# Kernel optimization log

Measured on AMD Instinct MI355X. Metric: run time of the kernel, lower is better.

## Reference

```python
import jax, jax.numpy as jnp
import numpy as np

N = 50000      # nodes
E = 800000     # edges per meta-path
P = 3          # meta-paths
IN = 128       # in_size
OUT = 64       # out_size per head
H = 4          # heads
HID = 128      # semantic-attention hidden
NEG_SLOPE = 0.2


def setup_inputs() -> dict:
    key = jax.random.key(0)
    ks = jax.random.split(key, 8)
    h = jax.random.normal(ks[0], (N, IN), jnp.float32)
    edges = jax.random.randint(ks[1], (P, 2, E), 0, N, dtype=jnp.int32)  # [P, (src,dst), E]
    fc_w = jax.random.normal(ks[2], (P, IN, H * OUT), jnp.float32) * 0.05
    attn_l = jax.random.normal(ks[3], (P, H, OUT), jnp.float32) * 0.05
    attn_r = jax.random.normal(ks[4], (P, H, OUT), jnp.float32) * 0.05
    w1 = jax.random.normal(ks[5], (H * OUT, HID), jnp.float32) * 0.05
    b1 = jnp.zeros((HID,), jnp.float32)
    w2 = jax.random.normal(ks[6], (HID,), jnp.float32) * 0.05
    return {"h": h, "edges": edges, "fc_w": fc_w, "attn_l": attn_l,
            "attn_r": attn_r, "w1": w1, "b1": b1, "w2": w2}


def _gat(h, edge, fc_w, al, ar):
    # One GATConv (DGL semantics, eval mode: dropout off, no residual/bias).
    src, dst = edge[0], edge[1]
    feat = (h @ fc_w).reshape(N, H, OUT)                 # [N,H,D]
    el = jnp.einsum('nhd,hd->nh', feat, al)              # [N,H]
    er = jnp.einsum('nhd,hd->nh', feat, ar)
    e = jax.nn.leaky_relu(el[src] + er[dst], NEG_SLOPE)  # [E,H]
    # edge softmax over incoming edges of each dst node
    m = jax.ops.segment_max(e, dst, num_segments=N)      # [N,H]
    m = jnp.where(jnp.isfinite(m), m, 0.0)               # empty segments -> 0
    ex = jnp.exp(e - m[dst])
    s = jax.ops.segment_sum(ex, dst, num_segments=N)     # [N,H]
    alpha = ex / s[dst]                                  # [E,H]
    msg = feat[src] * alpha[:, :, None]                  # [E,H,D]
    rst = jax.ops.segment_sum(msg, dst, num_segments=N)  # [N,H,D]
    return jax.nn.elu(rst).reshape(N, H * OUT)


def reference(h, edges, fc_w, attn_l, attn_r, w1, b1, w2):
    # per-meta-path GAT embeddings -> [N, P, H*OUT]
    z = jnp.stack([_gat(h, edges[i], fc_w[i], attn_l[i], attn_r[i])
                   for i in range(P)], axis=1)
    # semantic attention: Linear -> tanh -> Linear(no bias) -> softmax over P
    w = jnp.tanh(z @ w1 + b1) @ w2                       # [N,P]
    beta = jax.nn.softmax(w, axis=1)[:, :, None]         # [N,P,1]
    return (beta * z).sum(axis=1)                        # [N, H*OUT]
```

## Files before the change

### kernel.cpp

```cpp
#include <hip/hip_runtime.h>
#include <hip/hip_bf16.h>
#include <hip/hip_fp16.h>

#define N_NODES 50000
#define N_EDGES 800000
#define N_PATHS 3
#define IN_F    128
#define HO      256
#define N_HEADS 4
#define HID     128

#define BLK_PER_PATH 32
#define EDGES_PER_HB 25000
#define HIST_BLOCKS  (N_PATHS * BLK_PER_PATH)
#define NPACK        12500
#define FEAT_RB      782
#define SCAT_BLOCKS  2344
#define FEAT_ELEMS   ((size_t)N_NODES * HO)

typedef __bf16 bf16;
typedef __bf16 bf16x8 __attribute__((ext_vector_type(8)));
typedef float  f32x4  __attribute__((ext_vector_type(4)));
typedef unsigned short u16;
typedef unsigned char  u8;
typedef unsigned int   u32;

__global__ __launch_bounds__(256) void k_prep(const float* __restrict__ fc_w,
                                              bf16* __restrict__ fcwT) {
    int g = blockIdx.x * 256 + threadIdx.x;
    int p = g >> 15, r = g & 32767;
    int col = r & 255, k = r >> 8;
    fcwT[(size_t)p * 32768 + col * IN_F + k] = (bf16)fc_w[(size_t)p * 32768 + k * HO + col];
}

__global__ __launch_bounds__(256) void k_hist(const int* __restrict__ edges,
                                              u32* __restrict__ cnt32,
                                              u8* __restrict__ lrank) {
    __shared__ u32 hist[NPACK];
    const int b = blockIdx.x;
    const int p = b / BLK_PER_PATH, blk = b - p * BLK_PER_PATH;
    const int t = threadIdx.x;
    for (int i = t; i < NPACK; i += 256) hist[i] = 0;
    __syncthreads();

    const int* dstp = edges + (size_t)p * 2 * N_EDGES + N_EDGES + blk * EDGES_PER_HB;
    u8* lr = lrank + (size_t)p * N_EDGES + blk * EDGES_PER_HB;
    for (int q = t; q < EDGES_PER_HB / 4; q += 256) {
        int4 d4 = ((const int4*)dstp)[q];
        u32 o0 = atomicAdd(&hist[d4.x >> 2], 1u << ((d4.x & 3) * 8));
        u32 o1 = atomicAdd(&hist[d4.y >> 2], 1u << ((d4.y & 3) * 8));
        u32 o2 = atomicAdd(&hist[d4.z >> 2], 1u << ((d4.z & 3) * 8));
        u32 o3 = atomicAdd(&hist[d4.w >> 2], 1u << ((d4.w & 3) * 8));
        uchar4 r4;
        r4.x = (u8)(o0 >> ((d4.x & 3) * 8));
        r4.y = (u8)(o1 >> ((d4.y & 3) * 8));
        r4.z = (u8)(o2 >> ((d4.z & 3) * 8));
        r4.w = (u8)(o3 >> ((d4.w & 3) * 8));
        ((uchar4*)lr)[q] = r4;
    }
    __syncthreads();
    u32* out = cnt32 + (size_t)b * NPACK;
    for (int i = t; i < NPACK; i += 256) out[i] = hist[i];
}

__global__ __launch_bounds__(256) void k_base(u32* __restrict__ cnt32,
                                              int* __restrict__ deg) {
    int g = blockIdx.x * 256 + threadIdx.x;
    if (g >= N_PATHS * NPACK) return;
    int p = g / NPACK, q = g - p * NPACK;
    u32 s0 = 0, s1 = 0, s2 = 0, s3 = 0;
#pragma unroll
    for (int blk = 0; blk < BLK_PER_PATH; ++blk) {
        size_t idx = (size_t)(p * BLK_PER_PATH + blk) * NPACK + q;
        u32 c = cnt32[idx];
        cnt32[idx] = s0 | (s1 << 8) | (s2 << 16) | (s3 << 24);
        s0 += c & 0xff; s1 += (c >> 8) & 0xff; s2 += (c >> 16) & 0xff; s3 += c >> 24;
    }
    int4 d4 = {(int)s0, (int)s1, (int)s2, (int)s3};
    *(int4*)(deg + (size_t)p * N_NODES + 4 * q) = d4;
}

__global__ __launch_bounds__(1024) void k_scan(const int* __restrict__ deg,
                                               int* __restrict__ rowptr) {
    __shared__ int part[1024];
    const int p = blockIdx.x;
    const int* dg = deg + p * N_NODES;
    int* rp = rowptr + p * (N_NODES + 1);

    const int tid = threadIdx.x;
    const int CH = (N_NODES + 1023) / 1024;
    const int start = tid * CH;
    int s = 0;
    for (int i = 0; i < CH; ++i) { int idx = start + i; if (idx < N_NODES) s += dg[idx]; }
    part[tid] = s;
    __syncthreads();
    for (int off = 1; off < 1024; off <<= 1) {
        int v = (tid >= off) ? part[tid - off] : 0;
        __syncthreads();
        part[tid] += v;
        __syncthreads();
    }
    int excl = (tid == 0) ? 0 : part[tid - 1];
    for (int i = 0; i < CH; ++i) {
        int idx = start + i;
        if (idx < N_NODES) { rp[idx] = excl; excl += dg[idx]; }
    }
    if (tid == 1023) rp[N_NODES] = N_EDGES;
}

__device__ __forceinline__ void scatter_role(int b, const int* __restrict__ edges,
                                             const u8* __restrict__ lrank,
                                             const u32* __restrict__ cnt32,
                                             const int* __restrict__ rowptr,
                                             u16* __restrict__ csr) {
    int gt = b * 256 + threadIdx.x;
    if (gt >= (N_PATHS * N_EDGES) / 4) return;
    int base = gt * 4;
    int p = base / N_EDGES, e = base - p * N_EDGES;
    const int blk = e / EDGES_PER_HB;
    const int* ep = edges + (size_t)p * 2 * N_EDGES;
    int4 s4 = *(const int4*)(ep + e);
    int4 d4 = *(const int4*)(ep + N_EDGES + e);
    uchar4 r4 = *(const uchar4*)(lrank + base);
    const int* rp = rowptr + p * (N_NODES + 1);
    const u32* bb = cnt32 + (size_t)(p * BLK_PER_PATH + blk) * NPACK;
    u16* c = csr + (size_t)p * N_EDGES;
    int p0 = rp[d4.x] + ((bb[d4.x >> 2] >> ((d4.x & 3) * 8)) & 0xff) + r4.x;
    int p1 = rp[d4.y] + ((bb[d4.y >> 2] >> ((d4.y & 3) * 8)) & 0xff) + r4.y;
    int p2 = rp[d4.z] + ((bb[d4.z >> 2] >> ((d4.z & 3) * 8)) & 0xff) + r4.z;
    int p3 = rp[d4.w] + ((bb[d4.w >> 2] >> ((d4.w & 3) * 8)) & 0xff) + r4.w;
    c[p0] = (u16)s4.x; c[p1] = (u16)s4.y; c[p2] = (u16)s4.z; c[p3] = (u16)s4.w;
}

__device__ __forceinline__ void feat_role(int rb, const float* __restrict__ h,
                                          const bf16* __restrict__ fcwT,
                                          const float* __restrict__ al,
                                          const float* __restrict__ ar,
                                          __half* __restrict__ featAll,
                                          float* __restrict__ elAll,
                                          float* __restrict__ erAll) {
    const int t = threadIdx.x, w = t >> 6, l = t & 63, lo = l & 15, hi = l >> 4;
    const int arow = rb * 64 + w * 16 + lo;
    const int crow = rb * 64 + w * 16 + hi * 4;

    bf16x8 afr[4];
    if (arow < N_NODES) {
        const float* hp = h + (size_t)arow * IN_F;
#pragma unroll
        for (int ks = 0; ks < 4; ++ks) {
            float4 f0 = *(const float4*)(hp + ks * 32 + hi * 8);
            float4 f1 = *(const float4*)(hp + ks * 32 + hi * 8 + 4);
            bf16x8 a;
            a[0]=(bf16)f0.x; a[1]=(bf16)f0.y; a[2]=(bf16)f0.z; a[3]=(bf16)f0.w;
            a[4]=(bf16)f1.x; a[5]=(bf16)f1.y; a[6]=(bf16)f1.z; a[7]=(bf16)f1.w;
            afr[ks] = a;
        }
    } else {
#pragma unroll
        for (int ks = 0; ks < 4; ++ks) { bf16x8 a = {}; afr[ks] = a; }
    }

    for (int p = 0; p < N_PATHS; ++p) {
        __half* feat = featAll + (size_t)p * FEAT_ELEMS;
        const float* alp = al + p * HO;
        const float* arp = ar + p * HO;
        float* elA = elAll + (size_t)p * N_NODES * 4;
        float* erA = erAll + (size_t)p * N_NODES * 4;
#pragma unroll
        for (int ch = 0; ch < 2; ++ch) {
            const bf16* W = fcwT + (size_t)p * 32768 + (size_t)ch * 128 * IN_F;
            f32x4 acc[8];
#pragma unroll
            for (int c = 0; c < 8; ++c) { f32x4 zz = {0.f,0.f,0.f,0.f}; acc[c] = zz; }
#pragma unroll
            for (int ctl = 0; ctl < 8; ++ctl) {
                const bf16* wp = W + (size_t)(ctl * 16 + lo) * IN_F + hi * 8;
                f32x4 a = acc[ctl];
#pragma unroll
                for (int ks = 0; ks < 4; ++ks)
                    a = __builtin_amdgcn_mfma_f32_16x16x32_bf16(afr[ks], *(const bf16x8*)(wp + ks * 32), a, 0, 0, 0);
                acc[ctl] = a;
            }
            float elP[2][4] = {{0}}, erP[2][4] = {{0}};
#pragma unroll
            for (int ctl = 0; ctl < 8; ++ctl) {
                const int gcol = ch * 128 + ctl * 16 + lo;
                const float av = alp[gcol], bv = arp[gcol];
                const int hl = ctl >> 2;
#pragma unroll
                for (int rr = 0; rr < 4; ++rr) {
                    float v = acc[ctl][rr];
                    elP[hl][rr] = fmaf(v, av, elP[hl][rr]);
                    erP[hl][rr] = fmaf(v, bv, erP[hl][rr]);
                    if (crow + rr < N_NODES)
                        feat[(size_t)(crow + rr) * HO + gcol] = __float2half(v);
                }
            }
#pragma unroll
            for (int hl = 0; hl < 2; ++hl)
#pragma unroll
                for (int rr = 0; rr < 4; ++rr) {
                    float v = elP[hl][rr], u = erP[hl][rr];
#pragma unroll
                    for (int m = 1; m <= 8; m <<= 1) {
                        v += __shfl_xor(v, m, 64);
                        u += __shfl_xor(u, m, 64);
                    }
                    elP[hl][rr] = v; erP[hl][rr] = u;
                }
            if (lo == 0) {
#pragma unroll
                for (int rr = 0; rr < 4; ++rr) {
                    if (crow + rr < N_NODES) {
                        *(float2*)&elA[(crow + rr) * 4 + ch * 2] = make_float2(elP[0][rr], elP[1][rr]);
                        *(float2*)&erA[(crow + rr) * 4 + ch * 2] = make_float2(erP[0][rr], erP[1][rr]);
                    }
                }
            }
        }
    }
}

__global__ __launch_bounds__(256, 4) void k_fs(const int* __restrict__ edges,
                                               const u8* __restrict__ lrank,
                                               const u32* __restrict__ cnt32,
                                               const int* __restrict__ rowptr,
                                               u16* __restrict__ csr,
                                               const float* __restrict__ h,
                                               const bf16* __restrict__ fcwT,
                                               const float* __restrict__ al,
                                               const float* __restrict__ ar,
                                               __half* __restrict__ featAll,
                                               float* __restrict__ elAll,
                                               float* __restrict__ erAll) {
    const int bid = blockIdx.x;
    if (bid < SCAT_BLOCKS)
        scatter_role(bid, edges, lrank, cnt32, rowptr, csr);
    else
        feat_role(bid - SCAT_BLOCKS, h, fcwT, al, ar, featAll, elAll, erAll);
}

__global__ __launch_bounds__(256) void k_gather3(const u16* __restrict__ csrAll,
                                                 const int* __restrict__ rowptrAll,
                                                 const float4* __restrict__ elAll,
                                                 const float4* __restrict__ erAll,
                                                 const __half* __restrict__ featAll,
                                                 bf16* __restrict__ z) {
    __shared__ int     off_lds[4][64];
    __shared__ __half2 a_lds[4][64][4];
    const int pb = blockIdx.x;
    const int p  = pb / (N_NODES / 4);
    const int nb = pb - p * (N_NODES / 4);
    const u16*    csr    = csrAll + (size_t)p * N_EDGES;
    const int*    rowptr = rowptrAll + p * (N_NODES + 1);
    const float4* el4    = elAll + (size_t)p * N_NODES;
    const float4* er4    = erAll + (size_t)p * N_NODES;
    const __half* feat   = featAll + (size_t)p * FEAT_ELEMS;

    const int wid = threadIdx.x >> 6, l = threadIdx.x & 63;
    const int n = nb * 4 + wid;
    const int half = l >> 5, c = l & 31, hh = c >> 3;

    const int b0 = rowptr[n], b1 = rowptr[n + 1];
    const float4 er_n = er4[n];

    __half2 acc0 = __float2half2_rn(0.f), acc1 = acc0, acc2 = acc0, acc3 = acc0;
    float4 den = {0.f, 0.f, 0.f, 0.f};

    for (int base = b0; base < b1; base += 64) {
        const int cnt = min(64, b1 - base);
        if (l < cnt) {
            int sv = csr[base + l];
            off_lds[wid][l] = sv * HO;
            float4 e = el4[sv];
            float vx = e.x + er_n.x, vy = e.y + er_n.y,
                  vz = e.z + er_n.z, vw = e.w + er_n.w;
            vx = (vx >= 0.f) ? vx : 0.2f * vx;
            vy = (vy >= 0.f) ? vy : 0.2f * vy;
            vz = (vz >= 0.f) ? vz : 0.2f * vz;
            vw = (vw >= 0.f) ? vw : 0.2f * vw;
            float ex = __expf(vx), ey = __expf(vy), ez = __expf(vz), ew = __expf(vw);
            den.x += ex; den.y += ey; den.z += ez; den.w += ew;
            a_lds[wid][l][0] = __float2half2_rn(ex);
            a_lds[wid][l][1] = __float2half2_rn(ey);
            a_lds[wid][l][2] = __float2half2_rn(ez);
            a_lds[wid][l][3] = __float2half2_rn(ew);
        }
        for (int i2 = 0; i2 < cnt; i2 += 2) {
            const int e = i2 + half;
            if (e < cnt) {
                const int off = off_lds[wid][e];
                const __half2 a2 = a_lds[wid][e][hh];
                const uint4 u = *(const uint4*)(feat + off + c * 8);
                acc0 = __hfma2(__builtin_bit_cast(__half2, u.x), a2, acc0);
                acc1 = __hfma2(__builtin_bit_cast(__half2, u.y), a2, acc1);
                acc2 = __hfma2(__builtin_bit_cast(__half2, u.z), a2, acc2);
                acc3 = __hfma2(__builtin_bit_cast(__half2, u.w), a2, acc3);
            }
        }
    }

    float s[8];
    { float2 f0 = __half22float2(acc0), f1 = __half22float2(acc1),
             f2 = __half22float2(acc2), f3 = __half22float2(acc3);
      s[0]=f0.x; s[1]=f0.y; s[2]=f1.x; s[3]=f1.y; s[4]=f2.x; s[5]=f2.y; s[6]=f3.x; s[7]=f3.y; }
#pragma unroll
    for (int j = 0; j < 8; ++j) s[j] += __shfl_xor(s[j], 32, 64);
#pragma unroll
    for (int off = 32; off; off >>= 1) {
        den.x += __shfl_xor(den.x, off, 64);
        den.y += __shfl_xor(den.y, off, 64);
        den.z += __shfl_xor(den.z, off, 64);
        den.w += __shfl_xor(den.w, off, 64);
    }
    const float d = (hh == 0) ? den.x : (hh == 1) ? den.y : (hh == 2) ? den.z : den.w;
    const float inv = (d > 0.f) ? 1.f / d : 0.f;
    if (half == 0) {
        bf16x8 ov;
#pragma unroll
        for (int j = 0; j < 8; ++j) {
            float v = s[j] * inv;
            v = (v > 0.f) ? v : expm1f(v);
            ov[j] = (bf16)v;
        }
        *(bf16x8*)(z + (size_t)n * (N_PATHS * HO) + p * HO + c * 8) = ov;
    }
}

__global__ __launch_bounds__(256) void k_semout(const bf16* __restrict__ z,
                                                const float* __restrict__ w1,
                                                const float* __restrict__ b1,
                                                const float* __restrict__ w2,
                                                float* __restrict__ out) {
    __shared__ bf16  zs[48 * 264];
    __shared__ float psem[4][48];
    __shared__ float betas[16][4];

    const int t = threadIdx.x, w = t >> 6, l = t & 63;
    const int lo = l & 15, hi = l >> 4;
    const int n0 = blockIdx.x * 16;

    bf16x8 bfr[2][8];
#pragma unroll
    for (int ct = 0; ct < 2; ++ct) {
        const int j = (2 * w + ct) * 16 + lo;
#pragma unroll
        for (int s = 0; s < 8; ++s) {
            const int k0 = s * 32 + hi * 8;
            bf16x8 b;
#pragma unroll
            for (int i = 0; i < 8; ++i) b[i] = (bf16)w1[(k0 + i) * HID + j];
            bfr[ct][s] = b;
        }
    }

    const uint4* zg4 = (const uint4*)(z + (size_t)n0 * (N_PATHS * HO));
    for (int i = t; i < 1536; i += 256) {
        uint4 v = zg4[i];
        int r = i >> 5, cin = (i & 31) * 8;
        *(uint4*)&zs[r * 264 + cin] = v;
    }
    __syncthreads();

    f32x4 acc[2][3];
#pragma unroll
    for (int ct = 0; ct < 2; ++ct)
#pragma unroll
        for (int m = 0; m < 3; ++m) { f32x4 zz = {0.f,0.f,0.f,0.f}; acc[ct][m] = zz; }

    for (int s = 0; s < 8; ++s) {
#pragma unroll
        for (int m = 0; m < 3; ++m) {
            bf16x8 a = *(const bf16x8*)&zs[(m * 16 + lo) * 264 + s * 32 + hi * 8];
            acc[0][m] = __builtin_amdgcn_mfma_f32_16x16x32_bf16(a, bfr[0][s], acc[0][m], 0, 0, 0);
            acc[1][m] = __builtin_amdgcn_mfma_f32_16x16x32_bf16(a, bfr[1][s], acc[1][m], 0, 0, 0);
        }
    }

    const int j0 = (2 * w + 0) * 16 + lo;
    const int j1 = (2 * w + 1) * 16 + lo;
    const float b1_0 = b1[j0], w2_0 = w2[j0];
    const float b1_1 = b1[j1], w2_1 = w2[j1];
#pragma unroll
    for (int m = 0; m < 3; ++m) {
#pragma unroll
        for (int r = 0; r < 4; ++r) {
// ... 16 lines not shown
        float is = 1.f / (e0 + e1 + e2);
        betas[t][0] = e0 * is; betas[t][1] = e1 * is; betas[t][2] = e2 * is;
    }
    __syncthreads();
    for (int i = 0; i < 16; ++i) {
        float bb0 = betas[i][0], bb1 = betas[i][1], bb2 = betas[i][2];
        float o = bb0 * (float)zs[(3 * i + 0) * 264 + t]
                + bb1 * (float)zs[(3 * i + 1) * 264 + t]
                + bb2 * (float)zs[(3 * i + 2) * 264 + t];
        out[(size_t)(n0 + i) * HO + t] = o;
    }
}

static inline size_t align256(size_t x) { return (x + 255) & ~(size_t)255; }

extern "C" void kernel_launch(void* const* d_in, const int* in_sizes, int n_in,
                              void* d_out, int out_size, void* d_ws, size_t ws_size,
                              hipStream_t stream) {
    const float* h     = (const float*)d_in[0];
    const int*   edges = (const int*)d_in[1];
    const float* fc_w  = (const float*)d_in[2];
    const float* al    = (const float*)d_in[3];
    const float* ar    = (const float*)d_in[4];
    const float* w1    = (const float*)d_in[5];
    const float* b1    = (const float*)d_in[6];
    const float* w2    = (const float*)d_in[7];
    float* out = (float*)d_out;

    char* base = (char*)d_ws;
    size_t off = 0;
    auto carve = [&](size_t bytes) -> char* {
        char* p = base + off; off = align256(off + bytes); return p;
    };
    bf16*   zbuf   = (bf16*)carve((size_t)N_NODES * N_PATHS * HO * 2);
    __half* feat   = (__half*)carve((size_t)N_PATHS * FEAT_ELEMS * 2);
    bf16*   fcwT   = (bf16*)carve((size_t)N_PATHS * IN_F * HO * 2);
    float*  el     = (float*)carve((size_t)N_PATHS * N_NODES * 4 * 4);
    float*  er     = (float*)carve((size_t)N_PATHS * N_NODES * 4 * 4);
    int*    deg    = (int*)carve((size_t)N_PATHS * N_NODES * 4);
    int*    rowptr = (int*)carve((size_t)N_PATHS * (N_NODES + 1) * 4);
    u8*     lrank  = (u8*)carve((size_t)N_PATHS * N_EDGES);
    u16*    csr    = (u16*)carve((size_t)N_PATHS * N_EDGES * 2);
    u32*    cnt32  = (u32*)carve((size_t)HIST_BLOCKS * NPACK * 4);
    (void)ws_size; (void)in_sizes; (void)n_in; (void)out_size;

    k_prep<<<384, 256, 0, stream>>>(fc_w, fcwT);
    k_hist<<<HIST_BLOCKS, 256, 0, stream>>>(edges, cnt32, lrank);
    k_base<<<(N_PATHS * NPACK + 255) / 256, 256, 0, stream>>>(cnt32, deg);
    k_scan<<<N_PATHS, 1024, 0, stream>>>(deg, rowptr);
    k_fs<<<SCAT_BLOCKS + FEAT_RB, 256, 0, stream>>>(
        edges, lrank, cnt32, rowptr, csr, h, fcwT, al, ar, feat, el, er);
    k_gather3<<<N_PATHS * (N_NODES / 4), 256, 0, stream>>>(
        csr, rowptr, (const float4*)el, (const float4*)er, feat, zbuf);
    k_semout<<<N_NODES / 16, 256, 0, stream>>>(zbuf, w1, b1, w2, out);
}
```

Measured before the change: 492.3 us.

## Precompute edge attention in CSR scatter and co-schedule feature GEMM with histogram

The feature GEMM now runs in the same launch as the dst histogram instead of alongside the CSR scatter. The scatter kernel runs after the features exist. It computes each edge's leaky-relu exp weights and stores a 16-byte record (src offset plus fp16 weights) at the edge's CSR position. The gather kernel then reads these precomputed records and no longer does the random el/er lookups and exp itself. It also unrolls the aggregation loop to two edges per half-wave, for more loads in flight. The cost is scatter traffic of 16 B per edge instead of 2 B, and the 48 KB histogram LDS allocation is now shared with the feature blocks, which may reduce their occupancy.

Result: slower. 515.1 us (+4.6%).

```diff
diff --git a/kernel.cpp b/kernel.cpp
--- a/kernel.cpp
+++ b/kernel.cpp
@@ -25,6 +25,8 @@
 typedef unsigned char  u8;
 typedef unsigned int   u32;
 
+struct EdEnt { int off; __half2 a; };
+
 __global__ __launch_bounds__(256) void k_prep(const float* __restrict__ fc_w,
                                               bf16* __restrict__ fcwT) {
     int g = blockIdx.x * 256 + threadIdx.x;
@@ -33,11 +35,9 @@
     fcwT[(size_t)p * 32768 + col * IN_F + k] = (bf16)fc_w[(size_t)p * 32768 + k * HO + col];
 }
 
-__global__ __launch_bounds__(256) void k_hist(const int* __restrict__ edges,
-                                              u32* __restrict__ cnt32,
-                                              u8* __restrict__ lrank) {
-    __shared__ u32 hist[NPACK];
-    const int b = blockIdx.x;
+__device__ __forceinline__ void hist_role(int b, const int* __restrict__ edges,
+                                          u32* __restrict__ cnt32, u8* __restrict__ lrank,
+                                          u32* hist) {
     const int p = b / BLK_PER_PATH, blk = b - p * BLK_PER_PATH;
     const int t = threadIdx.x;
     for (int i = t; i < NPACK; i += 256) hist[i] = 0;
@@ -63,6 +63,113 @@
     for (int i = t; i < NPACK; i += 256) out[i] = hist[i];
 }
 
+__device__ __forceinline__ void feat_role(int rb, const float* __restrict__ h,
+                                          const bf16* __restrict__ fcwT,
+                                          const float* __restrict__ al,
+                                          const float* __restrict__ ar,
+                                          __half* __restrict__ featAll,
+                                          float* __restrict__ elAll,
+                                          float* __restrict__ erAll) {
+    const int t = threadIdx.x, w = t >> 6, l = t & 63, lo = l & 15, hi = l >> 4;
+    const int arow = rb * 64 + w * 16 + lo;
+    const int crow = rb * 64 + w * 16 + hi * 4;
+
+    bf16x8 afr[4];
+    if (arow < N_NODES) {
+        const float* hp = h + (size_t)arow * IN_F;
+#pragma unroll
+        for (int ks = 0; ks < 4; ++ks) {
+            float4 f0 = *(const float4*)(hp + ks * 32 + hi * 8);
+            float4 f1 = *(const float4*)(hp + ks * 32 + hi * 8 + 4);
+            bf16x8 a;
+            a[0]=(bf16)f0.x; a[1]=(bf16)f0.y; a[2]=(bf16)f0.z; a[3]=(bf16)f0.w;
+            a[4]=(bf16)f1.x; a[5]=(bf16)f1.y; a[6]=(bf16)f1.z; a[7]=(bf16)f1.w;
+            afr[ks] = a;
+        }
+    } else {
+#pragma unroll
+        for (int ks = 0; ks < 4; ++ks) { bf16x8 a = {}; afr[ks] = a; }
+    }
+
+    for (int p = 0; p < N_PATHS; ++p) {
+        __half* feat = featAll + (size_t)p * FEAT_ELEMS;
+        const float* alp = al + p * HO;
+        const float* arp = ar + p * HO;
+        float* elA = elAll + (size_t)p * N_NODES * 4;
+        float* erA = erAll + (size_t)p * N_NODES * 4;
+#pragma unroll
+        for (int ch = 0; ch < 2; ++ch) {
+            const bf16* W = fcwT + (size_t)p * 32768 + (size_t)ch * 128 * IN_F;
+            f32x4 acc[8];
+#pragma unroll
+            for (int c = 0; c < 8; ++c) { f32x4 zz = {0.f,0.f,0.f,0.f}; acc[c] = zz; }
+#pragma unroll
+            for (int ctl = 0; ctl < 8; ++ctl) {
+                const bf16* wp = W + (size_t)(ctl * 16 + lo) * IN_F + hi * 8;
+                f32x4 a = acc[ctl];
+#pragma unroll
+                for (int ks = 0; ks < 4; ++ks)
+                    a = __builtin_amdgcn_mfma_f32_16x16x32_bf16(afr[ks], *(const bf16x8*)(wp + ks * 32), a, 0, 0, 0);
+                acc[ctl] = a;
+            }
+            float elP[2][4] = {{0}}, erP[2][4] = {{0}};
+#pragma unroll
+            for (int ctl = 0; ctl < 8; ++ctl) {
+                const int gcol = ch * 128 + ctl * 16 + lo;
+                const float av = alp[gcol], bv = arp[gcol];
+                const int hl = ctl >> 2;
+#pragma unroll
+                for (int rr = 0; rr < 4; ++rr) {
+                    float v = acc[ctl][rr];
+                    elP[hl][rr] = fmaf(v, av, elP[hl][rr]);
+                    erP[hl][rr] = fmaf(v, bv, erP[hl][rr]);
+                    if (crow + rr < N_NODES)
+                        feat[(size_t)(crow + rr) * HO + gcol] = __float2half(v);
+                }
+            }
+#pragma unroll
+            for (int hl = 0; hl < 2; ++hl)
+#pragma unroll
+                for (int rr = 0; rr < 4; ++rr) {
+                    float v = elP[hl][rr], u = erP[hl][rr];
+#pragma unroll
+                    for (int m = 1; m <= 8; m <<= 1) {
+                        v += __shfl_xor(v, m, 64);
+                        u += __shfl_xor(u, m, 64);
+                    }
+                    elP[hl][rr] = v; erP[hl][rr] = u;
+                }
+            if (lo == 0) {
+#pragma unroll
+                for (int rr = 0; rr < 4; ++rr) {
+                    if (crow + rr < N_NODES) {
+                        *(float2*)&elA[(crow + rr) * 4 + ch * 2] = make_float2(elP[0][rr], elP[1][rr]);
+                        *(float2*)&erA[(crow + rr) * 4 + ch * 2] = make_float2(erP[0][rr], erP[1][rr]);
+                    }
+                }
+            }
+        }
+    }
+}
+
+__global__ __launch_bounds__(256) void k_hf(const int* __restrict__ edges,
+                                            u32* __restrict__ cnt32,
+                                            u8* __restrict__ lrank,
+                                            const float* __restrict__ h,
+                                            const bf16* __restrict__ fcwT,
+                                            const float* __restrict__ al,
+                                            const float* __restrict__ ar,
+                                            __half* __restrict__ featAll,
+                                            float* __restrict__ elAll,
+                                            float* __restrict__ erAll) {
+    __shared__ u32 hist[NPACK];
+    const int bid = blockIdx.x;
+    if (bid < HIST_BLOCKS)
+        hist_role(bid, edges, cnt32, lrank, hist);
+    else
+        feat_role(bid - HIST_BLOCKS, h, fcwT, al, ar, featAll, elAll, erAll);
+}
+
 __global__ __launch_bounds__(256) void k_base(u32* __restrict__ cnt32,
                                               int* __restrict__ deg) {
     int g = blockIdx.x * 256 + threadIdx.x;
@@ -108,12 +215,14 @@
     if (tid == 1023) rp[N_NODES] = N_EDGES;
 }
 
-__device__ __forceinline__ void scatter_role(int b, const int* __restrict__ edges,
-                                             const u8* __restrict__ lrank,
-                                             const u32* __restrict__ cnt32,
-                                             const int* __restrict__ rowptr,
-                                             u16* __restrict__ csr) {
-    int gt = b * 256 + threadIdx.x;
+__global__ __launch_bounds__(256) void k_scata(const int* __restrict__ edges,
+                                               const u8* __restrict__ lrank,
+                                               const u32* __restrict__ cnt32,
+                                               const int* __restrict__ rowptr,
+                                               const float4* __restrict__ elAll,
+                                               const float4* __restrict__ erAll,
+                                               uint4* __restrict__ csrE) {
+    int gt = blockIdx.x * 256 + threadIdx.x;
     if (gt >= (N_PATHS * N_EDGES) / 4) return;
     int base = gt * 4;
     int p = base / N_EDGES, e = base - p * N_EDGES;
@@ -124,145 +233,51 @@
     uchar4 r4 = *(const uchar4*)(lrank + base);
     const int* rp = rowptr + p * (N_NODES + 1);
     const u32* bb = cnt32 + (size_t)(p * BLK_PER_PATH + blk) * NPACK;
-    u16* c = csr + (size_t)p * N_EDGES;
-    int p0 = rp[d4.x] + ((bb[d4.x >> 2] >> ((d4.x & 3) * 8)) & 0xff) + r4.x;
-    int p1 = rp[d4.y] + ((bb[d4.y >> 2] >> ((d4.y & 3) * 8)) & 0xff) + r4.y;
-    int p2 = rp[d4.z] + ((bb[d4.z >> 2] >> ((d4.z & 3) * 8)) & 0xff) + r4.z;
-    int p3 = rp[d4.w] + ((bb[d4.w >> 2] >> ((d4.w & 3) * 8)) & 0xff) + r4.w;
-    c[p0] = (u16)s4.x; c[p1] = (u16)s4.y; c[p2] = (u16)s4.z; c[p3] = (u16)s4.w;
-}
-
-__device__ __forceinline__ void feat_role(int rb, const float* __restrict__ h,
-                                          const bf16* __restrict__ fcwT,
-                                          const float* __restrict__ al,
-                                          const float* __restrict__ ar,
-                                          __half* __restrict__ featAll,
-                                          float* __restrict__ elAll,
-                                          float* __restrict__ erAll) {
-    const int t = threadIdx.x, w = t >> 6, l = t & 63, lo = l & 15, hi = l >> 4;
-    const int arow = rb * 64 + w * 16 + lo;
-    const int crow = rb * 64 + w * 16 + hi * 4;
-
-    bf16x8 afr[4];
-    if (arow < N_NODES) {
-        const float* hp = h + (size_t)arow * IN_F;
-#pragma unroll
-        for (int ks = 0; ks < 4; ++ks) {
-            float4 f0 = *(const float4*)(hp + ks * 32 + hi * 8);
-            float4 f1 = *(const float4*)(hp + ks * 32 + hi * 8 + 4);
-            bf16x8 a;
-            a[0]=(bf16)f0.x; a[1]=(bf16)f0.y; a[2]=(bf16)f0.z; a[3]=(bf16)f0.w;
-            a[4]=(bf16)f1.x; a[5]=(bf16)f1.y; a[6]=(bf16)f1.z; a[7]=(bf16)f1.w;
-            afr[ks] = a;
-        }
-    } else {
-#pragma unroll
-        for (int ks = 0; ks < 4; ++ks) { bf16x8 a = {}; afr[ks] = a; }
-    }
-
-    for (int p = 0; p < N_PATHS; ++p) {
-        __half* feat = featAll + (size_t)p * FEAT_ELEMS;
-        const float* alp = al + p * HO;
-        const float* arp = ar + p * HO;
-        float* elA = elAll + (size_t)p * N_NODES * 4;
-        float* erA = erAll + (size_t)p * N_NODES * 4;
-#pragma unroll
-        for (int ch = 0; ch < 2; ++ch) {
-            const bf16* W = fcwT + (size_t)p * 32768 + (size_t)ch * 128 * IN_F;
-            f32x4 acc[8];
-#pragma unroll
-            for (int c = 0; c < 8; ++c) { f32x4 zz = {0.f,0.f,0.f,0.f}; acc[c] = zz; }
-#pragma unroll
-            for (int ctl = 0; ctl < 8; ++ctl) {
-                const bf16* wp = W + (size_t)(ctl * 16 + lo) * IN_F + hi * 8;
-                f32x4 a = acc[ctl];
-#pragma unroll
-                for (int ks = 0; ks < 4; ++ks)
-                    a = __builtin_amdgcn_mfma_f32_16x16x32_bf16(afr[ks], *(const bf16x8*)(wp + ks * 32), a, 0, 0, 0);
-                acc[ctl] = a;
-            }
-            float elP[2][4] = {{0}}, erP[2][4] = {{0}};
-#pragma unroll
-            for (int ctl = 0; ctl < 8; ++ctl) {
-                const int gcol = ch * 128 + ctl * 16 + lo;
-                const float av = alp[gcol], bv = arp[gcol];
-                const int hl = ctl >> 2;
-#pragma unroll
-                for (int rr = 0; rr < 4; ++rr) {
-                    float v = acc[ctl][rr];
-                    elP[hl][rr] = fmaf(v, av, elP[hl][rr]);
-                    erP[hl][rr] = fmaf(v, bv, erP[hl][rr]);
-                    if (crow + rr < N_NODES)
-                        feat[(size_t)(crow + rr) * HO + gcol] = __float2half(v);
-                }
-            }
-#pragma unroll
-            for (int hl = 0; hl < 2; ++hl)
-#pragma unroll
-                for (int rr = 0; rr < 4; ++rr) {
-                    float v = elP[hl][rr], u = erP[hl][rr];
-#pragma unroll
-                    for (int m = 1; m <= 8; m <<= 1) {
-                        v += __shfl_xor(v, m, 64);
-                        u += __shfl_xor(u, m, 64);
-                    }
-                    elP[hl][rr] = v; erP[hl][rr] = u;
-                }
-            if (lo == 0) {
-#pragma unroll
-                for (int rr = 0; rr < 4; ++rr) {
-                    if (crow + rr < N_NODES) {
-                        *(float2*)&elA[(crow + rr) * 4 + ch * 2] = make_float2(elP[0][rr], elP[1][rr]);
-                        *(float2*)&erA[(crow + rr) * 4 + ch * 2] = make_float2(erP[0][rr], erP[1][rr]);
-                    }
-                }
-            }
-        }
-    }
-}
-
-__global__ __launch_bounds__(256, 4) void k_fs(const int* __restrict__ edges,
-                                               const u8* __restrict__ lrank,
-                                               const u32* __restrict__ cnt32,
-                                               const int* __restrict__ rowptr,
-                                               u16* __restrict__ csr,
-                                               const float* __restrict__ h,
-                                               const bf16* __restrict__ fcwT,
-                                               const float* __restrict__ al,
-                                               const float* __restrict__ ar,
-                                               __half* __restrict__ featAll,
-                                               float* __restrict__ elAll,
-                                               float* __restrict__ erAll) {
-    const int bid = blockIdx.x;
-    if (bid < SCAT_BLOCKS)
-        scatter_role(bid, edges, lrank, cnt32, rowptr, csr);
-    else
-        feat_role(bid - SCAT_BLOCKS, h, fcwT, al, ar, featAll, elAll, erAll);
-}
-
-__global__ __launch_bounds__(256) void k_gather3(const u16* __restrict__ csrAll,
+    const float4* el4 = elAll + (size_t)p * N_NODES;
+    const float4* er4 = erAll + (size_t)p * N_NODES;
+    uint4* cE = csrE + (size_t)p * N_EDGES;
+
+    int ss[4] = {s4.x, s4.y, s4.z, s4.w};
+    int dd[4] = {d4.x, d4.y, d4.z, d4.w};
+    int rr[4] = {r4.x, r4.y, r4.z, r4.w};
+#pragma unroll
+    for (int j = 0; j < 4; ++j) {
+        const int s = ss[j], d = dd[j];
+        const int pos = rp[d] + (int)((bb[d >> 2] >> ((d & 3) * 8)) & 0xff) + rr[j];
+        float4 a = el4[s], b = er4[d];
+        float vx = a.x + b.x, vy = a.y + b.y, vz = a.z + b.z, vw = a.w + b.w;
+        vx = (vx >= 0.f) ? vx : 0.2f * vx;
+        vy = (vy >= 0.f) ? vy : 0.2f * vy;
+        vz = (vz >= 0.f) ? vz : 0.2f * vz;
+        vw = (vw >= 0.f) ? vw : 0.2f * vw;
+        __half2 h01 = __floats2half2_rn(__expf(vx), __expf(vy));
+        __half2 h23 = __floats2half2_rn(__expf(vz), __expf(vw));
+        uint4 entry;
+        entry.x = (u32)(s * HO);
+        entry.y = __builtin_bit_cast(u32, h01);
+        entry.z = __builtin_bit_cast(u32, h23);
+        entry.w = 0;
+        cE[pos] = entry;
+    }
+}
+
+__global__ __launch_bounds__(256) void k_gather3(const uint4* __restrict__ csrEAll,
                                                  const int* __restrict__ rowptrAll,
-                                                 const float4* __restrict__ elAll,
-                                                 const float4* __restrict__ erAll,
                                                  const __half* __restrict__ featAll,
                                                  bf16* __restrict__ z) {
-    __shared__ int     off_lds[4][64];
-    __shared__ __half2 a_lds[4][64][4];
+    __shared__ EdEnt ed[4][64][4];
     const int pb = blockIdx.x;
     const int p  = pb / (N_NODES / 4);
     const int nb = pb - p * (N_NODES / 4);
-    const u16*    csr    = csrAll + (size_t)p * N_EDGES;
-    const int*    rowptr = rowptrAll + p * (N_NODES + 1);
-    const float4* el4    = elAll + (size_t)p * N_NODES;
-    const float4* er4    = erAll + (size_t)p * N_NODES;
-    const __half* feat   = featAll + (size_t)p * FEAT_ELEMS;
+    const uint4* cE    = csrEAll + (size_t)p * N_EDGES;
+    const int* rowptr  = rowptrAll + p * (N_NODES + 1);
+    const __half* feat = featAll + (size_t)p * FEAT_ELEMS;
 
     const int wid = threadIdx.x >> 6, l = threadIdx.x & 63;
     const int n = nb * 4 + wid;
     const int half = l >> 5, c = l & 31, hh = c >> 3;
 
     const int b0 = rowptr[n], b1 = rowptr[n + 1];
-    const float4 er_n = er4[n];
 
     __half2 acc0 = __float2half2_rn(0.f), acc1 = acc0, acc2 = acc0, acc3 = acc0;
     float4 den = {0.f, 0.f, 0.f, 0.f};
@@ -270,32 +285,42 @@
     for (int base = b0; base < b1; base += 64) {
         const int cnt = min(64, b1 - base);
         if (l < cnt) {
-            int sv = csr[base + l];
-            off_lds[wid][l] = sv * HO;
-            float4 e = el4[sv];
-            float vx = e.x + er_n.x, vy = e.y + er_n.y,
-                  vz = e.z + er_n.z, vw = e.w + er_n.w;
-            vx = (vx >= 0.f) ? vx : 0.2f * vx;
-            vy = (vy >= 0.f) ? vy : 0.2f * vy;
-            vz = (vz >= 0.f) ? vz : 0.2f * vz;
-            vw = (vw >= 0.f) ? vw : 0.2f * vw;
-            float ex = __expf(vx), ey = __expf(vy), ez = __expf(vz), ew = __expf(vw);
-            den.x += ex; den.y += ey; den.z += ez; den.w += ew;
-            a_lds[wid][l][0] = __float2half2_rn(ex);
-            a_lds[wid][l][1] = __float2half2_rn(ey);
-            a_lds[wid][l][2] = __float2half2_rn(ez);
-            a_lds[wid][l][3] = __float2half2_rn(ew);
-        }
-        for (int i2 = 0; i2 < cnt; i2 += 2) {
+            uint4 m = cE[base + l];
+            __half2 h01 = __builtin_bit_cast(__half2, m.y);
+            __half2 h23 = __builtin_bit_cast(__half2, m.z);
+            float2 f01 = __half22float2(h01);
+            float2 f23 = __half22float2(h23);
+            den.x += f01.x; den.y += f01.y; den.z += f23.x; den.w += f23.y;
+            EdEnt* ep = ed[wid][l];
+            ep[0].off = (int)m.x; ep[0].a = __half2half2(__low2half(h01));
+            ep[1].off = (int)m.x; ep[1].a = __half2half2(__high2half(h01));
+            ep[2].off = (int)m.x; ep[2].a = __half2half2(__low2half(h23));
+            ep[3].off = (int)m.x; ep[3].a = __half2half2(__high2half(h23));
+        }
+        int i2 = 0;
+        for (; i2 + 4 <= cnt; i2 += 4) {
+            EdEnt e1 = ed[wid][i2 + half][hh];
+            EdEnt e2 = ed[wid][i2 + 2 + half][hh];
+            const uint4 u1 = *(const uint4*)(feat + e1.off + c * 8);
+            const uint4 u2 = *(const uint4*)(feat + e2.off + c * 8);
+            acc0 = __hfma2(__builtin_bit_cast(__half2, u1.x), e1.a, acc0);
+            acc1 = __hfma2(__builtin_bit_cast(__half2, u1.y), e1.a, acc1);
+            acc2 = __hfma2(__builtin_bit_cast(__half2, u1.z), e1.a, acc2);
+            acc3 = __hfma2(__builtin_bit_cast(__half2, u1.w), e1.a, acc3);
+            acc0 = __hfma2(__builtin_bit_cast(__half2, u2.x), e2.a, acc0);
+            acc1 = __hfma2(__builtin_bit_cast(__half2, u2.y), e2.a, acc1);
+            acc2 = __hfma2(__builtin_bit_cast(__half2, u2.z), e2.a, acc2);
+            acc3 = __hfma2(__builtin_bit_cast(__half2, u2.w), e2.a, acc3);
+        }
+        for (; i2 < cnt; i2 += 2) {
             const int e = i2 + half;
             if (e < cnt) {
-                const int off = off_lds[wid][e];
-                const __half2 a2 = a_lds[wid][e][hh];
-                const uint4 u = *(const uint4*)(feat + off + c * 8);
-                acc0 = __hfma2(__builtin_bit_cast(__half2, u.x), a2, acc0);
-                acc1 = __hfma2(__builtin_bit_cast(__half2, u.y), a2, acc1);
-                acc2 = __hfma2(__builtin_bit_cast(__half2, u.z), a2, acc2);
-                acc3 = __hfma2(__builtin_bit_cast(__half2, u.w), a2, acc3);
+                EdEnt e1 = ed[wid][e][hh];
+                const uint4 u = *(const uint4*)(feat + e1.off + c * 8);
+                acc0 = __hfma2(__builtin_bit_cast(__half2, u.x), e1.a, acc0);
+                acc1 = __hfma2(__builtin_bit_cast(__half2, u.y), e1.a, acc1);
+                acc2 = __hfma2(__builtin_bit_cast(__half2, u.z), e1.a, acc2);
+                acc3 = __hfma2(__builtin_bit_cast(__half2, u.w), e1.a, acc3);
             }
         }
     }
@@ -436,23 +461,23 @@
     };
     bf16*   zbuf   = (bf16*)carve((size_t)N_NODES * N_PATHS * HO * 2);
     __half* feat   = (__half*)carve((size_t)N_PATHS * FEAT_ELEMS * 2);
+    uint4*  csrE   = (uint4*)carve((size_t)N_PATHS * N_EDGES * 16);
     bf16*   fcwT   = (bf16*)carve((size_t)N_PATHS * IN_F * HO * 2);
     float*  el     = (float*)carve((size_t)N_PATHS * N_NODES * 4 * 4);
     float*  er     = (float*)carve((size_t)N_PATHS * N_NODES * 4 * 4);
     int*    deg    = (int*)carve((size_t)N_PATHS * N_NODES * 4);
     int*    rowptr = (int*)carve((size_t)N_PATHS * (N_NODES + 1) * 4);
     u8*     lrank  = (u8*)carve((size_t)N_PATHS * N_EDGES);
-    u16*    csr    = (u16*)carve((size_t)N_PATHS * N_EDGES * 2);
     u32*    cnt32  = (u32*)carve((size_t)HIST_BLOCKS * NPACK * 4);
     (void)ws_size; (void)in_sizes; (void)n_in; (void)out_size;
 
     k_prep<<<384, 256, 0, stream>>>(fc_w, fcwT);
-    k_hist<<<HIST_BLOCKS, 256, 0, stream>>>(edges, cnt32, lrank);
+    k_hf<<<HIST_BLOCKS + FEAT_RB, 256, 0, stream>>>(
+        edges, cnt32, lrank, h, fcwT, al, ar, feat, el, er);
     k_base<<<(N_PATHS * NPACK + 255) / 256, 256, 0, stream>>>(cnt32, deg);
     k_scan<<<N_PATHS, 1024, 0, stream>>>(deg, rowptr);
-    k_fs<<<SCAT_BLOCKS + FEAT_RB, 256, 0, stream>>>(
-        edges, lrank, cnt32, rowptr, csr, h, fcwT, al, ar, feat, el, er);
-    k_gather3<<<N_PATHS * (N_NODES / 4), 256, 0, stream>>>(
-        csr, rowptr, (const float4*)el, (const float4*)er, feat, zbuf);
+    k_scata<<<SCAT_BLOCKS, 256, 0, stream>>>(
+        edges, lrank, cnt32, rowptr, (const float4*)el, (const float4*)er, csrE);
+    k_gather3<<<N_PATHS * (N_NODES / 4), 256, 0, stream>>>(csrE, rowptr, feat, zbuf);
     k_semout<<<N_NODES / 16, 256, 0, stream>>>(zbuf, w1, b1, w2, out);
 }
```

## Restructure pipeline: fuse histogram with feature GEMM, overlap per-path scatter with gather

Applied to the files above, without the earlier changes.

The histogram pass now runs in the same launch as the feature projection, so both become independent blocks of one kernel. The CSR scatter for path p+1 now runs in the same launch as the aggregation for path p, split into per-path kernels that pipeline the scatter and gather stages. The gather inner loop is unrolled to issue two feature loads per lane per iteration, and its LDS attention layout is transposed. w1 is pre-transposed to bf16 in the prep kernel so semout can use vector loads. The cost is more launches, and the hist role's 50KB of shared memory may reduce occupancy of the feature blocks.

New measurement: 486.9 us. No clear change (-1.1%).

```diff
diff --git a/kernel.cpp b/kernel.cpp
--- a/kernel.cpp
+++ b/kernel.cpp
@@ -15,7 +15,8 @@
 #define HIST_BLOCKS  (N_PATHS * BLK_PER_PATH)
 #define NPACK        12500
 #define FEAT_RB      782
-#define SCAT_BLOCKS  2344
+#define SCAT_PP      782
+#define GATH_PP      12500
 #define FEAT_ELEMS   ((size_t)N_NODES * HO)
 
 typedef __bf16 bf16;
@@ -26,18 +27,26 @@
 typedef unsigned int   u32;
 
 __global__ __launch_bounds__(256) void k_prep(const float* __restrict__ fc_w,
-                                              bf16* __restrict__ fcwT) {
+                                              const float* __restrict__ w1,
+                                              bf16* __restrict__ fcwT,
+                                              bf16* __restrict__ w1T) {
     int g = blockIdx.x * 256 + threadIdx.x;
-    int p = g >> 15, r = g & 32767;
-    int col = r & 255, k = r >> 8;
-    fcwT[(size_t)p * 32768 + col * IN_F + k] = (bf16)fc_w[(size_t)p * 32768 + k * HO + col];
-}
-
-__global__ __launch_bounds__(256) void k_hist(const int* __restrict__ edges,
-                                              u32* __restrict__ cnt32,
-                                              u8* __restrict__ lrank) {
-    __shared__ u32 hist[NPACK];
-    const int b = blockIdx.x;
+    if (g < N_PATHS * IN_F * HO) {
+        int p = g >> 15, r = g & 32767;
+        int col = r & 255, k = r >> 8;
+        fcwT[(size_t)p * 32768 + col * IN_F + k] = (bf16)fc_w[(size_t)p * 32768 + k * HO + col];
+    } else {
+        int gg = g - N_PATHS * IN_F * HO;
+        if (gg < HO * HID) {
+            int k = gg & 255, j = gg >> 8;
+            w1T[(size_t)j * HO + k] = (bf16)w1[(size_t)k * HID + j];
+        }
+    }
+}
+
+__device__ __forceinline__ void hist_role(int b, const int* __restrict__ edges,
+                                          u32* __restrict__ cnt32, u8* __restrict__ lrank,
+                                          u32* hist) {
     const int p = b / BLK_PER_PATH, blk = b - p * BLK_PER_PATH;
     const int t = threadIdx.x;
     for (int i = t; i < NPACK; i += 256) hist[i] = 0;
@@ -63,75 +72,6 @@
     for (int i = t; i < NPACK; i += 256) out[i] = hist[i];
 }
 
-__global__ __launch_bounds__(256) void k_base(u32* __restrict__ cnt32,
-                                              int* __restrict__ deg) {
-    int g = blockIdx.x * 256 + threadIdx.x;
-    if (g >= N_PATHS * NPACK) return;
-    int p = g / NPACK, q = g - p * NPACK;
-    u32 s0 = 0, s1 = 0, s2 = 0, s3 = 0;
-#pragma unroll
-    for (int blk = 0; blk < BLK_PER_PATH; ++blk) {
-        size_t idx = (size_t)(p * BLK_PER_PATH + blk) * NPACK + q;
-        u32 c = cnt32[idx];
-        cnt32[idx] = s0 | (s1 << 8) | (s2 << 16) | (s3 << 24);
-        s0 += c & 0xff; s1 += (c >> 8) & 0xff; s2 += (c >> 16) & 0xff; s3 += c >> 24;
-    }
-    int4 d4 = {(int)s0, (int)s1, (int)s2, (int)s3};
-    *(int4*)(deg + (size_t)p * N_NODES + 4 * q) = d4;
-}
-
-__global__ __launch_bounds__(1024) void k_scan(const int* __restrict__ deg,
-                                               int* __restrict__ rowptr) {
-    __shared__ int part[1024];
-    const int p = blockIdx.x;
-    const int* dg = deg + p * N_NODES;
-    int* rp = rowptr + p * (N_NODES + 1);
-
-    const int tid = threadIdx.x;
-    const int CH = (N_NODES + 1023) / 1024;
-    const int start = tid * CH;
-    int s = 0;
-    for (int i = 0; i < CH; ++i) { int idx = start + i; if (idx < N_NODES) s += dg[idx]; }
-    part[tid] = s;
-    __syncthreads();
-    for (int off = 1; off < 1024; off <<= 1) {
-        int v = (tid >= off) ? part[tid - off] : 0;
-        __syncthreads();
-        part[tid] += v;
-        __syncthreads();
-    }
-    int excl = (tid == 0) ? 0 : part[tid - 1];
-    for (int i = 0; i < CH; ++i) {
-        int idx = start + i;
-        if (idx < N_NODES) { rp[idx] = excl; excl += dg[idx]; }
-    }
-    if (tid == 1023) rp[N_NODES] = N_EDGES;
-}
-
-__device__ __forceinline__ void scatter_role(int b, const int* __restrict__ edges,
-                                             const u8* __restrict__ lrank,
-                                             const u32* __restrict__ cnt32,
-                                             const int* __restrict__ rowptr,
-                                             u16* __restrict__ csr) {
-    int gt = b * 256 + threadIdx.x;
-    if (gt >= (N_PATHS * N_EDGES) / 4) return;
-    int base = gt * 4;
-    int p = base / N_EDGES, e = base - p * N_EDGES;
-    const int blk = e / EDGES_PER_HB;
-    const int* ep = edges + (size_t)p * 2 * N_EDGES;
-    int4 s4 = *(const int4*)(ep + e);
-    int4 d4 = *(const int4*)(ep + N_EDGES + e);
-    uchar4 r4 = *(const uchar4*)(lrank + base);
-    const int* rp = rowptr + p * (N_NODES + 1);
-    const u32* bb = cnt32 + (size_t)(p * BLK_PER_PATH + blk) * NPACK;
-    u16* c = csr + (size_t)p * N_EDGES;
-    int p0 = rp[d4.x] + ((bb[d4.x >> 2] >> ((d4.x & 3) * 8)) & 0xff) + r4.x;
-    int p1 = rp[d4.y] + ((bb[d4.y >> 2] >> ((d4.y & 3) * 8)) & 0xff) + r4.y;
-    int p2 = rp[d4.z] + ((bb[d4.z >> 2] >> ((d4.z & 3) * 8)) & 0xff) + r4.z;
-    int p3 = rp[d4.w] + ((bb[d4.w >> 2] >> ((d4.w & 3) * 8)) & 0xff) + r4.w;
-    c[p0] = (u16)s4.x; c[p1] = (u16)s4.y; c[p2] = (u16)s4.z; c[p3] = (u16)s4.w;
-}
-
 __device__ __forceinline__ void feat_role(int rb, const float* __restrict__ h,
                                           const bf16* __restrict__ fcwT,
                                           const float* __restrict__ al,
@@ -221,57 +161,119 @@
     }
 }
 
-__global__ __launch_bounds__(256, 4) void k_fs(const int* __restrict__ edges,
-                                               const u8* __restrict__ lrank,
-                                               const u32* __restrict__ cnt32,
-                                               const int* __restrict__ rowptr,
-                                               u16* __restrict__ csr,
-                                               const float* __restrict__ h,
-                                               const bf16* __restrict__ fcwT,
-                                               const float* __restrict__ al,
-                                               const float* __restrict__ ar,
-                                               __half* __restrict__ featAll,
-                                               float* __restrict__ elAll,
-                                               float* __restrict__ erAll) {
+__global__ __launch_bounds__(256) void k_hf(const int* __restrict__ edges,
+                                            u32* __restrict__ cnt32,
+                                            u8* __restrict__ lrank,
+                                            const float* __restrict__ h,
+                                            const bf16* __restrict__ fcwT,
+                                            const float* __restrict__ al,
+                                            const float* __restrict__ ar,
+                                            __half* __restrict__ featAll,
+                                            float* __restrict__ elAll,
+                                            float* __restrict__ erAll) {
+    __shared__ u32 hist[NPACK];
     const int bid = blockIdx.x;
-    if (bid < SCAT_BLOCKS)
-        scatter_role(bid, edges, lrank, cnt32, rowptr, csr);
+    if (bid < HIST_BLOCKS)
+        hist_role(bid, edges, cnt32, lrank, hist);
     else
-        feat_role(bid - SCAT_BLOCKS, h, fcwT, al, ar, featAll, elAll, erAll);
-}
-
-__global__ __launch_bounds__(256) void k_gather3(const u16* __restrict__ csrAll,
-                                                 const int* __restrict__ rowptrAll,
-                                                 const float4* __restrict__ elAll,
-                                                 const float4* __restrict__ erAll,
-                                                 const __half* __restrict__ featAll,
-                                                 bf16* __restrict__ z) {
-    __shared__ int     off_lds[4][64];
-    __shared__ __half2 a_lds[4][64][4];
-    const int pb = blockIdx.x;
-    const int p  = pb / (N_NODES / 4);
-    const int nb = pb - p * (N_NODES / 4);
+        feat_role(bid - HIST_BLOCKS, h, fcwT, al, ar, featAll, elAll, erAll);
+}
+
+__global__ __launch_bounds__(256) void k_base(u32* __restrict__ cnt32,
+                                              int* __restrict__ deg) {
+    int g = blockIdx.x * 256 + threadIdx.x;
+    if (g >= N_PATHS * NPACK) return;
+    int p = g / NPACK, q = g - p * NPACK;
+    u32 s0 = 0, s1 = 0, s2 = 0, s3 = 0;
+#pragma unroll
+    for (int blk = 0; blk < BLK_PER_PATH; ++blk) {
+        size_t idx = (size_t)(p * BLK_PER_PATH + blk) * NPACK + q;
+        u32 c = cnt32[idx];
+        cnt32[idx] = s0 | (s1 << 8) | (s2 << 16) | (s3 << 24);
+        s0 += c & 0xff; s1 += (c >> 8) & 0xff; s2 += (c >> 16) & 0xff; s3 += c >> 24;
+    }
+    int4 d4 = {(int)s0, (int)s1, (int)s2, (int)s3};
+    *(int4*)(deg + (size_t)p * N_NODES + 4 * q) = d4;
+}
+
+__global__ __launch_bounds__(1024) void k_scan(const int* __restrict__ deg,
+                                               int* __restrict__ rowptr) {
+    __shared__ int part[1024];
+    const int p = blockIdx.x;
+    const int* dg = deg + p * N_NODES;
+    int* rp = rowptr + p * (N_NODES + 1);
+
+    const int tid = threadIdx.x;
+    const int CH = (N_NODES + 1023) / 1024;
+    const int start = tid * CH;
+    int s = 0;
+    for (int i = 0; i < CH; ++i) { int idx = start + i; if (idx < N_NODES) s += dg[idx]; }
+    part[tid] = s;
+    __syncthreads();
+    for (int off = 1; off < 1024; off <<= 1) {
+        int v = (tid >= off) ? part[tid - off] : 0;
+        __syncthreads();
+        part[tid] += v;
+        __syncthreads();
+    }
+    int excl = (tid == 0) ? 0 : part[tid - 1];
+    for (int i = 0; i < CH; ++i) {
+        int idx = start + i;
+        if (idx < N_NODES) { rp[idx] = excl; excl += dg[idx]; }
+    }
+    if (tid == 1023) rp[N_NODES] = N_EDGES;
+}
+
+__device__ __forceinline__ void scatter_role(int b, int p, const int* __restrict__ edges,
+                                             const u8* __restrict__ lrank,
+                                             const u32* __restrict__ cnt32,
+                                             const int* __restrict__ rowptr,
+                                             u16* __restrict__ csrAll) {
+    int e = (b * 256 + threadIdx.x) * 4;
+    if (e >= N_EDGES) return;
+    const int blk = e / EDGES_PER_HB;
+    const int* ep = edges + (size_t)p * 2 * N_EDGES;
+    int4 s4 = *(const int4*)(ep + e);
+    int4 d4 = *(const int4*)(ep + N_EDGES + e);
+    uchar4 r4 = *(const uchar4*)(lrank + (size_t)p * N_EDGES + e);
+    const int* rp = rowptr + p * (N_NODES + 1);
+    const u32* bb = cnt32 + (size_t)(p * BLK_PER_PATH + blk) * NPACK;
+    u16* c = csrAll + (size_t)p * N_EDGES;
+    int p0 = rp[d4.x] + (int)((bb[d4.x >> 2] >> ((d4.x & 3) * 8)) & 0xff) + r4.x;
+    int p1 = rp[d4.y] + (int)((bb[d4.y >> 2] >> ((d4.y & 3) * 8)) & 0xff) + r4.y;
+    int p2 = rp[d4.z] + (int)((bb[d4.z >> 2] >> ((d4.z & 3) * 8)) & 0xff) + r4.z;
+    int p3 = rp[d4.w] + (int)((bb[d4.w >> 2] >> ((d4.w & 3) * 8)) & 0xff) + r4.w;
+    c[p0] = (u16)s4.x; c[p1] = (u16)s4.y; c[p2] = (u16)s4.z; c[p3] = (u16)s4.w;
+}
+
+__device__ __forceinline__ void gather_role(int nb, int p,
+                                            const u16* __restrict__ csrAll,
+                                            const int* __restrict__ rowptrAll,
+                                            const float4* __restrict__ elAll,
+                                            const float4* __restrict__ erAll,
+                                            const __half* __restrict__ featAll,
+                                            bf16* __restrict__ z,
+                                            u32 (*s_off)[64], __half2 (*s_ad)[4][66]) {
+    const int t = threadIdx.x, w = t >> 6, l = t & 63;
+    const int half = l >> 5, c = l & 31, hh = c >> 3;
+    const int n = nb * 4 + w;
+
     const u16*    csr    = csrAll + (size_t)p * N_EDGES;
     const int*    rowptr = rowptrAll + p * (N_NODES + 1);
     const float4* el4    = elAll + (size_t)p * N_NODES;
-    const float4* er4    = erAll + (size_t)p * N_NODES;
     const __half* feat   = featAll + (size_t)p * FEAT_ELEMS;
 
-    const int wid = threadIdx.x >> 6, l = threadIdx.x & 63;
-    const int n = nb * 4 + wid;
-    const int half = l >> 5, c = l & 31, hh = c >> 3;
-
-    const int b0 = rowptr[n], b1 = rowptr[n + 1];
-    const float4 er_n = er4[n];
+    const int b0 = rowptr[n], b1e = rowptr[n + 1];
+    const float4 er_n = (erAll + (size_t)p * N_NODES)[n];
 
     __half2 acc0 = __float2half2_rn(0.f), acc1 = acc0, acc2 = acc0, acc3 = acc0;
     float4 den = {0.f, 0.f, 0.f, 0.f};
 
-    for (int base = b0; base < b1; base += 64) {
-        const int cnt = min(64, b1 - base);
+    for (int base = b0; base < b1e; base += 64) {
+        const int cnt = min(64, b1e - base);
         if (l < cnt) {
             int sv = csr[base + l];
-            off_lds[wid][l] = sv * HO;
+            s_off[w][l] = (u32)(sv * HO);
             float4 e = el4[sv];
             float vx = e.x + er_n.x, vy = e.y + er_n.y,
                   vz = e.z + er_n.z, vw = e.w + er_n.w;
@@ -281,21 +283,37 @@
             vw = (vw >= 0.f) ? vw : 0.2f * vw;
             float ex = __expf(vx), ey = __expf(vy), ez = __expf(vz), ew = __expf(vw);
             den.x += ex; den.y += ey; den.z += ez; den.w += ew;
-            a_lds[wid][l][0] = __float2half2_rn(ex);
-            a_lds[wid][l][1] = __float2half2_rn(ey);
-            a_lds[wid][l][2] = __float2half2_rn(ez);
-            a_lds[wid][l][3] = __float2half2_rn(ew);
-        }
-        for (int i2 = 0; i2 < cnt; i2 += 2) {
+            s_ad[w][0][l] = __float2half2_rn(ex);
+            s_ad[w][1][l] = __float2half2_rn(ey);
+            s_ad[w][2][l] = __float2half2_rn(ez);
+            s_ad[w][3][l] = __float2half2_rn(ew);
+        }
+        int i2 = 0;
+        for (; i2 + 4 <= cnt; i2 += 4) {
+            const int e1 = i2 + half, e2 = i2 + 2 + half;
+            u32 o1 = s_off[w][e1], o2 = s_off[w][e2];
+            __half2 a1 = s_ad[w][hh][e1], a2v = s_ad[w][hh][e2];
+            const uint4 u1 = *(const uint4*)(feat + o1 + c * 8);
+            const uint4 u2 = *(const uint4*)(feat + o2 + c * 8);
+            acc0 = __hfma2(__builtin_bit_cast(__half2, u1.x), a1, acc0);
+            acc1 = __hfma2(__builtin_bit_cast(__half2, u1.y), a1, acc1);
+            acc2 = __hfma2(__builtin_bit_cast(__half2, u1.z), a1, acc2);
+            acc3 = __hfma2(__builtin_bit_cast(__half2, u1.w), a1, acc3);
+            acc0 = __hfma2(__builtin_bit_cast(__half2, u2.x), a2v, acc0);
+            acc1 = __hfma2(__builtin_bit_cast(__half2, u2.y), a2v, acc1);
+            acc2 = __hfma2(__builtin_bit_cast(__half2, u2.z), a2v, acc2);
+            acc3 = __hfma2(__builtin_bit_cast(__half2, u2.w), a2v, acc3);
+        }
+        for (; i2 < cnt; i2 += 2) {
             const int e = i2 + half;
             if (e < cnt) {
-                const int off = off_lds[wid][e];
-                const __half2 a2 = a_lds[wid][e][hh];
-                const uint4 u = *(const uint4*)(feat + off + c * 8);
-                acc0 = __hfma2(__builtin_bit_cast(__half2, u.x), a2, acc0);
-                acc1 = __hfma2(__builtin_bit_cast(__half2, u.y), a2, acc1);
-                acc2 = __hfma2(__builtin_bit_cast(__half2, u.z), a2, acc2);
-                acc3 = __hfma2(__builtin_bit_cast(__half2, u.w), a2, acc3);
+                u32 o1 = s_off[w][e];
+                __half2 a1 = s_ad[w][hh][e];
+                const uint4 u = *(const uint4*)(feat + o1 + c * 8);
+                acc0 = __hfma2(__builtin_bit_cast(__half2, u.x), a1, acc0);
+                acc1 = __hfma2(__builtin_bit_cast(__half2, u.y), a1, acc1);
+                acc2 = __hfma2(__builtin_bit_cast(__half2, u.z), a1, acc2);
+                acc3 = __hfma2(__builtin_bit_cast(__half2, u.w), a1, acc3);
             }
         }
     }
@@ -327,8 +345,28 @@
     }
 }
 
+__global__ __launch_bounds__(256) void k_gs(int gp, int sp,
+                                            const int* __restrict__ edges,
+                                            const u8* __restrict__ lrank,
+                                            const u32* __restrict__ cnt32,
+                                            const int* __restrict__ rowptr,
+                                            u16* __restrict__ csr,
+                                            const float4* __restrict__ el,
+                                            const float4* __restrict__ er,
+                                            const __half* __restrict__ feat,
+                                            bf16* __restrict__ z) {
+    __shared__ u32     s_off[4][64];
+    __shared__ __half2 s_ad[4][4][66];
+    const int bid = blockIdx.x;
+    if (bid < SCAT_PP) {
+        if (sp >= 0) scatter_role(bid, sp, edges, lrank, cnt32, rowptr, csr);
+    } else if (gp >= 0) {
+        gather_role(bid - SCAT_PP, gp, csr, rowptr, el, er, feat, z, s_off, s_ad);
+    }
+}
+
 __global__ __launch_bounds__(256) void k_semout(const bf16* __restrict__ z,
-                                                const float* __restrict__ w1,
+                                                const bf16* __restrict__ w1T,
                                                 const float* __restrict__ b1,
                                                 const float* __restrict__ w2,
                                                 float* __restrict__ out) {
@@ -345,13 +383,8 @@
     for (int ct = 0; ct < 2; ++ct) {
         const int j = (2 * w + ct) * 16 + lo;
 #pragma unroll
-        for (int s = 0; s < 8; ++s) {
-            const int k0 = s * 32 + hi * 8;
-            bf16x8 b;
-#pragma unroll
-            for (int i = 0; i < 8; ++i) b[i] = (bf16)w1[(k0 + i) * HID + j];
-            bfr[ct][s] = b;
-        }
+        for (int s = 0; s < 8; ++s)
+            bfr[ct][s] = *(const bf16x8*)(w1T + (size_t)j * HO + s * 32 + hi * 8);
     }
 
     const uint4* zg4 = (const uint4*)(z + (size_t)n0 * (N_PATHS * HO));
@@ -434,25 +467,31 @@
     auto carve = [&](size_t bytes) -> char* {
         char* p = base + off; off = align256(off + bytes); return p;
     };
+    __half* feat   = (__half*)carve((size_t)N_PATHS * FEAT_ELEMS * 2);
     bf16*   zbuf   = (bf16*)carve((size_t)N_NODES * N_PATHS * HO * 2);
-    __half* feat   = (__half*)carve((size_t)N_PATHS * FEAT_ELEMS * 2);
+    u16*    csr    = (u16*)carve((size_t)N_PATHS * N_EDGES * 2);
     bf16*   fcwT   = (bf16*)carve((size_t)N_PATHS * IN_F * HO * 2);
+    bf16*   w1T    = (bf16*)carve((size_t)HO * HID * 2);
     float*  el     = (float*)carve((size_t)N_PATHS * N_NODES * 4 * 4);
     float*  er     = (float*)carve((size_t)N_PATHS * N_NODES * 4 * 4);
     int*    deg    = (int*)carve((size_t)N_PATHS * N_NODES * 4);
     int*    rowptr = (int*)carve((size_t)N_PATHS * (N_NODES + 1) * 4);
     u8*     lrank  = (u8*)carve((size_t)N_PATHS * N_EDGES);
-    u16*    csr    = (u16*)carve((size_t)N_PATHS * N_EDGES * 2);
     u32*    cnt32  = (u32*)carve((size_t)HIST_BLOCKS * NPACK * 4);
     (void)ws_size; (void)in_sizes; (void)n_in; (void)out_size;
 
-    k_prep<<<384, 256, 0, stream>>>(fc_w, fcwT);
-    k_hist<<<HIST_BLOCKS, 256, 0, stream>>>(edges, cnt32, lrank);
+    k_prep<<<512, 256, 0, stream>>>(fc_w, w1, fcwT, w1T);
+    k_hf<<<HIST_BLOCKS + FEAT_RB, 256, 0, stream>>>(
+        edges, cnt32, lrank, h, fcwT, al, ar, feat, el, er);
     k_base<<<(N_PATHS * NPACK + 255) / 256, 256, 0, stream>>>(cnt32, deg);
     k_scan<<<N_PATHS, 1024, 0, stream>>>(deg, rowptr);
-    k_fs<<<SCAT_BLOCKS + FEAT_RB, 256, 0, stream>>>(
-        edges, lrank, cnt32, rowptr, csr, h, fcwT, al, ar, feat, el, er);
-    k_gather3<<<N_PATHS * (N_NODES / 4), 256, 0, stream>>>(
-        csr, rowptr, (const float4*)el, (const float4*)er, feat, zbuf);
-    k_semout<<<N_NODES / 16, 256, 0, stream>>>(zbuf, w1, b1, w2, out);
-}
+    k_gs<<<SCAT_PP, 256, 0, stream>>>(-1, 0, edges, lrank, cnt32, rowptr, csr,
+                                      (const float4*)el, (const float4*)er, feat, zbuf);
+    k_gs<<<SCAT_PP + GATH_PP, 256, 0, stream>>>(0, 1, edges, lrank, cnt32, rowptr, csr,
+                                      (const float4*)el, (const float4*)er, feat, zbuf);
+    k_gs<<<SCAT_PP + GATH_PP, 256, 0, stream>>>(1, 2, edges, lrank, cnt32, rowptr, csr,
+                                      (const float4*)el, (const float4*)er, feat, zbuf);
+    k_gs<<<SCAT_PP + GATH_PP, 256, 0, stream>>>(2, -1, edges, lrank, cnt32, rowptr, csr,
+                                      (const float4*)el, (const float4*)er, feat, zbuf);
+    k_semout<<<N_NODES / 16, 256, 0, stream>>>(zbuf, w1T, b1, w2, out);
+}
```
